# Kernel optimization log

Hardware: AMD Instinct MI355X
Metric: run time of the kernel (lower is better)

Reference implementation:

```python
import jax, jax.numpy as jnp
import numpy as np

NP_CONST = 48.0  # Np in the original code


def dft_matrices(freq=48, time=512):
    # A[t, f] = exp(-2j*pi*t*f/time)/sqrt(time), split into re/im, shape [time, freq]
    t = np.arange(time)[:, None]
    f = np.arange(freq)[None, :]
    ang = -2.0 * np.pi * t * f / time
    scale = 1.0 / np.sqrt(time)
    return (np.cos(ang) * scale).astype(np.float32), (np.sin(ang) * scale).astype(np.float32)


def _mm(xr, xi, wr, wi):
    # complex matmul: (xr + i xi) @ (wr + i wi)
    return xr @ wr - xi @ wi, xr @ wi + xi @ wr


def _act(R, sigma, theta):
    # scaled soft-threshold (standard LAMP shrinkage); returns f and df/dR
    lam = theta[0] * sigma
    mag = jnp.abs(R)
    shr = jnp.maximum(mag - lam, 0.0)
    f = theta[1] * jnp.sign(R) * shr
    df = theta[1] * (mag > lam).astype(R.dtype)
    return f, df


def setup_inputs() -> dict:
    key = jax.random.key(0)
    L, B = 8, 8192
    dre, dim = dft_matrices(48, 512)
    u = jax.random.normal(key, (B, 48, 2), dtype=jnp.float32)
    # per-layer params initialized to the DFT matrices (as in LAMP_layer.__init__)
    A_re = jnp.broadcast_to(jnp.asarray(dre), (L, 512, 48)).copy()
    A_im = jnp.broadcast_to(jnp.asarray(dim), (L, 512, 48)).copy()
    theta = jnp.broadcast_to(jnp.array([1.0, 1.0, -1.0], dtype=jnp.float32), (L, 3)).copy()
    return {"u": u, "A_re": A_re, "A_im": A_im, "theta": theta,
            "DFT_re": jnp.asarray(dre), "DFT_im": jnp.asarray(dim)}


def _lamp_forward(u, A_re, A_im, theta, DFT_re, DFT_im):
    u_re, u_im = u[:, :, 0], u[:, :, 1]          # [B, 48]
    B = u_re.shape[0]
    z_re, z_im = u_re, u_im
    H_re = jnp.zeros((B, 512), dtype=u.dtype)
    H_im = jnp.zeros((B, 512), dtype=u.dtype)

    def layer(carry, params):
        z_re, z_im, H_re, H_im = carry
        Are, Aim, th = params                      # [512,48], [512,48], [3]
        # Z = z @ A.T : [B,48] x [48,512]
        Z_re, Z_im = _mm(z_re, z_im, Are.T, Aim.T)
        R_re = H_re + Z_re
        R_im = H_im + Z_im
        sigma = jnp.sqrt(jnp.sum(z_re * z_re) + jnp.sum(z_im * z_im)) / jnp.sqrt(NP_CONST)
        Hn_re, d_re = _act(R_re, sigma, th)
        Hn_im, d_im = _act(R_im, sigma, th)
        b_re = d_re.sum() / NP_CONST
        b_im = d_im.sum() / NP_CONST
        # h_hat = H_hat @ A : [B,512] x [512,48]
        h_re, h_im = _mm(Hn_re, Hn_im, Are, Aim)
        zn_re = u_re - h_re + b_re * z_re
        zn_im = u_im - h_im + b_im * z_im
        return (zn_re, zn_im, Hn_re, Hn_im), None

    (z_re, z_im, H_re, H_im), _ = jax.lax.scan(layer, (z_re, z_im, H_re, H_im),
                                               (A_re, A_im, theta))
    h_re, h_im = _mm(H_re, H_im, DFT_re, DFT_im)   # [B, 48]
    return jnp.stack((h_re, h_im), axis=2)          # [B, 48, 2]


def reference(u, A_re, A_im, theta, DFT_re, DFT_im):
    return _lamp_forward(u, A_re, A_im, theta, DFT_re, DFT_im)
```

## Files before the change

kernel.cpp:

```cpp
#include <hip/hip_runtime.h>
#include <hip/hip_bf16.h>
#include <math.h>

#define B_   8192
#define F_   48
#define T_   512
#define L_   8
#define NBLK 256
#define THR  512
#define NW   8
#define RPB  32
#define HST  520
#define ZS   52

typedef unsigned short ushort_t;
typedef unsigned int   uint_t;
typedef __attribute__((ext_vector_type(8))) short short8;
typedef __attribute__((ext_vector_type(4))) float f32x4;

#define MFMA(a,b,c) __builtin_amdgcn_mfma_f32_16x16x32_bf16(a,b,c,0,0,0)

__device__ inline ushort_t f2bf(float x) {
    __hip_bfloat16 h = __float2bfloat16(x);
    return *reinterpret_cast<ushort_t*>(&h);
}
__device__ inline short8 negbf(short8 v) {
    short8 r;
    #pragma unroll
    for (int i = 0; i < 8; ++i) r[i] = v[i] ^ (short)0x8000;
    return r;
}
__device__ inline short8 pack8(float4 a, float4 b) {
    short8 r;
    r[0]=(short)f2bf(a.x); r[1]=(short)f2bf(a.y); r[2]=(short)f2bf(a.z); r[3]=(short)f2bf(a.w);
    r[4]=(short)f2bf(b.x); r[5]=(short)f2bf(b.y); r[6]=(short)f2bf(b.z); r[7]=(short)f2bf(b.w);
    return r;
}

__device__ inline void bar_add(uint_t* cnt) {
    __hip_atomic_fetch_add(cnt, 1u, __ATOMIC_RELEASE, __HIP_MEMORY_SCOPE_AGENT);
}
__device__ inline void bar_wait(uint_t* cnt, uint_t tgt) {
    if (threadIdx.x == 0) {
        while (__hip_atomic_load(cnt, __ATOMIC_RELAXED, __HIP_MEMORY_SCOPE_AGENT) < tgt)
            __builtin_amdgcn_s_sleep(2);
        (void)__hip_atomic_load(cnt, __ATOMIC_ACQUIRE, __HIP_MEMORY_SCOPE_AGENT);
    }
    __syncthreads();
}
__device__ inline float aload(const float* p) {
    return __hip_atomic_load(p, __ATOMIC_RELAXED, __HIP_MEMORY_SCOPE_AGENT);
}
__device__ inline void afadd(float* p, float v) {
    (void)__hip_atomic_fetch_add(p, v, __ATOMIC_RELAXED, __HIP_MEMORY_SCOPE_AGENT);
}

__global__ __launch_bounds__(256) void k_pre(
    const float* __restrict__ Ar, const float* __restrict__ Ai,
    const float* __restrict__ Dr, const float* __restrict__ Di,
    ushort_t* __restrict__ Afr, ushort_t* __restrict__ Afi,
    ushort_t* __restrict__ Atr, ushort_t* __restrict__ Ati,
    ushort_t* __restrict__ Dfr, ushort_t* __restrict__ Dfi,
    float* __restrict__ slots, uint_t* __restrict__ cnt)
{
    const int gt = blockIdx.x * 256 + threadIdx.x;
    const int gs = gridDim.x * 256;
    if (gt == 0) *cnt = 0u;
    if (gt < 32) slots[gt] = 0.f;
    for (int idx = gt; idx < L_ * 32768; idx += gs) {
        int j = idx & 7, rest = idx >> 3;
        int mm = rest & 15; rest >>= 4;
        int qq = rest & 3;  rest >>= 2;
        int k2 = rest & 1;  rest >>= 1;
        int tile = rest & 31;
        int l = rest >> 5;
        int t = tile * 16 + mm, k = k2 * 32 + qq * 8 + j;
        float vr = 0.f, vi = 0.f;
        if (k < 48) { int g = l * 24576 + t * 48 + k; vr = Ar[g]; vi = Ai[g]; }
        Afr[idx] = f2bf(vr); Afi[idx] = f2bf(vi);
    }
    for (int idx = gt; idx < L_ * 24576; idx += gs) {
        int j = idx & 7, rest = idx >> 3;
        int mm = rest & 15; rest >>= 4;
        int qq = rest & 3;  rest >>= 2;
        int ks = rest & 15; rest >>= 4;
        int ft = rest % 3;
        int l = rest / 3;
        int f = ft * 16 + mm, k = ks * 32 + qq * 8 + j;
        int g = l * 24576 + k * 48 + f;
        Atr[idx] = f2bf(Ar[g]); Ati[idx] = f2bf(Ai[g]);
    }
    for (int idx = gt; idx < 24576; idx += gs) {
        int j = idx & 7, rest = idx >> 3;
        int mm = rest & 15; rest >>= 4;
        int qq = rest & 3;  rest >>= 2;
        int ks = rest & 15;
        int ft = rest >> 4;
        int f = ft * 16 + mm, k = ks * 32 + qq * 8 + j;
        Dfr[idx] = f2bf(Dr[k * 48 + f]); Dfi[idx] = f2bf(Di[k * 48 + f]);
    }
}

__global__ __launch_bounds__(THR, 2) void k_lamp(
    const float* __restrict__ u,
    const ushort_t* __restrict__ Afr, const ushort_t* __restrict__ Afi,
    const ushort_t* __restrict__ Atr, const ushort_t* __restrict__ Ati,
    const ushort_t* __restrict__ Dfr, const ushort_t* __restrict__ Dfi,
    const float* __restrict__ th,
    float* slots, uint_t* cnt,
    float* __restrict__ out)
{
    extern __shared__ char dyn[];
    float*    pR   = (float*)dyn;
    float*    pI   = pR + 8 * 3 * 16 * 17;
    float*    zreL = pI + 8 * 3 * 16 * 17;
    float*    zimL = zreL + RPB * ZS;
    float*    red8 = zimL + RPB * ZS;
    ushort_t* HreL = (ushort_t*)(red8 + 16);
    ushort_t* HimL = HreL + RPB * HST;

    const int tid = threadIdx.x, blk = blockIdx.x;
    const int row0 = blk * RPB;
    const int wave = tid >> 6, lane = tid & 63;
    const int quad = lane >> 4, m = lane & 15;
    const int rows16 = (wave >> 2) * 16;
    const int rt = wave >> 2, kq = wave & 3;
    const float2* u2 = (const float2*)u;
    float* sigS = slots;
    float* brS  = slots + 8;
    float* biS  = slots + 16;
    uint_t tgt = 0;

    f32x4 hR[8], hI[8];
    #pragma unroll
    for (int ct = 0; ct < 8; ++ct) { hR[ct] = (f32x4){0,0,0,0}; hI[ct] = (f32x4){0,0,0,0}; }

    float acc = 0.f;
    #pragma unroll
    for (int k3 = 0; k3 < 3; ++k3) {
        int j = tid + k3 * THR;
        int r = j / 48, c = j - r * 48;
        float2 v = u2[(row0 + r) * 48 + c];
        zreL[r * ZS + c] = v.x; zimL[r * ZS + c] = v.y;
        acc += v.x * v.x + v.y * v.y;
    }
    #pragma unroll
    for (int s = 32; s > 0; s >>= 1) acc += __shfl_xor(acc, s, 64);
    __syncthreads();
    if ((tid & 63) == 0) red8[tid >> 6] = acc;
    __syncthreads();
    if (tid == 0) {
        float t = 0.f;
        #pragma unroll
        for (int w = 0; w < NW; ++w) t += red8[w];
        afadd(&sigS[0], t); bar_add(cnt);
    }
    tgt += NBLK;

    for (int l = 0; l < L_; ++l) {
        const float* zpr = zreL + (rows16 + m) * ZS;
        const float* zpi = zimL + (rows16 + m) * ZS;
        short8 zr0 = pack8(*(const float4*)(zpr + quad * 8), *(const float4*)(zpr + quad * 8 + 4));
        short8 zi0 = pack8(*(const float4*)(zpi + quad * 8), *(const float4*)(zpi + quad * 8 + 4));
        short8 zr1 = {0,0,0,0,0,0,0,0}, zi1 = {0,0,0,0,0,0,0,0};
        if (quad < 2) {
            zr1 = pack8(*(const float4*)(zpr + 32 + quad * 8), *(const float4*)(zpr + 36 + quad * 8));
            zi1 = pack8(*(const float4*)(zpi + 32 + quad * 8), *(const float4*)(zpi + 36 + quad * 8));
        }
        short8 zin0 = negbf(zi0), zin1 = negbf(zi1);

        const ushort_t* Aflr = Afr + (size_t)l * 32768;
        const ushort_t* Afli = Afi + (size_t)l * 32768;
        #pragma unroll
        for (int ct = 0; ct < 8; ++ct) {
            const int tile = (wave & 3) * 8 + ct;
            const ushort_t* rp = Aflr + (size_t)(tile * 2) * 512 + lane * 8;
            const ushort_t* ip = Afli + (size_t)(tile * 2) * 512 + lane * 8;
            short8 ar0 = *(const short8*)rp;
            short8 ar1 = *(const short8*)(rp + 512);
            short8 ai0 = *(const short8*)ip;
            short8 ai1 = *(const short8*)(ip + 512);
            hR[ct] = MFMA(zr0, ar0, hR[ct]);
            hR[ct] = MFMA(zr1, ar1, hR[ct]);
            hR[ct] = MFMA(zin0, ai0, hR[ct]);
            hR[ct] = MFMA(zin1, ai1, hR[ct]);
            hI[ct] = MFMA(zr0, ai0, hI[ct]);
            hI[ct] = MFMA(zr1, ai1, hI[ct]);
            hI[ct] = MFMA(zi0, ar0, hI[ct]);
            hI[ct] = MFMA(zi1, ar1, hI[ct]);
        }

        bar_wait(cnt, tgt);
        const float lam = th[l * 3] * sqrtf(aload(&sigS[l]) * (1.0f / 48.0f));
        const float th1 = th[l * 3 + 1];

        float cr = 0.f, ci = 0.f;
        #pragma unroll
        for (int ct = 0; ct < 8; ++ct) {
            const int t = ((wave & 3) * 8 + ct) * 16 + m;
            #pragma unroll
            for (int reg = 0; reg < 4; ++reg) {
                const int lr = rows16 + quad * 4 + reg;
                float Rr = hR[ct][reg], Ri = hI[ct][reg];
                float mr = fabsf(Rr), mi = fabsf(Ri);
                float fr = th1 * copysignf(fmaxf(mr - lam, 0.f), Rr);
                float fi = th1 * copysignf(fmaxf(mi - lam, 0.f), Ri);
                cr += (mr > lam) ? 1.f : 0.f;
                ci += (mi > lam) ? 1.f : 0.f;
                hR[ct][reg] = fr; hI[ct][reg] = fi;
                HreL[lr * HST + t] = f2bf(fr);
                HimL[lr * HST + t] = f2bf(fi);
            }
        }

        if (l == L_ - 1) { __syncthreads(); break; }

        #pragma unroll
        for (int s = 32; s > 0; s >>= 1) { cr += __shfl_xor(cr, s, 64); ci += __shfl_xor(ci, s, 64); }
        __syncthreads();
        if ((tid & 63) == 0) { red8[tid >> 6] = cr; red8[8 + (tid >> 6)] = ci; }
        __syncthreads();
        if (tid == 0) {
            float tr = 0.f, tii = 0.f;
            #pragma unroll
            for (int w = 0; w < NW; ++w) { tr += red8[w]; tii += red8[8 + w]; }
            afadd(&brS[l], tr); afadd(&biS[l], tii); bar_add(cnt);
        }
        tgt += NBLK;

        const ushort_t* Atlr = Atr + (size_t)l * 24576;
        const ushort_t* Atli = Ati + (size_t)l * 24576;
        f32x4 aR[3], aI[3];
        #pragma unroll
        for (int q = 0; q < 3; ++q) { aR[q] = (f32x4){0,0,0,0}; aI[q] = (f32x4){0,0,0,0}; }
        #pragma unroll
        for (int ks = 0; ks < 4; ++ks) {
            const int ksa = kq * 4 + ks;
            const int k0 = ksa * 32 + quad * 8;
            short8 hr = *(const short8*)&HreL[(rt * 16 + m) * HST + k0];
            short8 hi = *(const short8*)&HimL[(rt * 16 + m) * HST + k0];
            short8 hin = negbf(hi);
            #pragma unroll
            for (int ft = 0; ft < 3; ++ft) {
                short8 br = *(const short8*)(Atlr + (size_t)((ft * 16 + ksa) * 64 + lane) * 8);
                short8 bi = *(const short8*)(Atli + (size_t)((ft * 16 + ksa) * 64 + lane) * 8);
                aR[ft] = MFMA(hr, br, aR[ft]);
                aR[ft] = MFMA(hin, bi, aR[ft]);
                aI[ft] = MFMA(hr, bi, aI[ft]);
                aI[ft] = MFMA(hi, br, aI[ft]);
            }
        }
        #pragma unroll
        for (int ft = 0; ft < 3; ++ft) {
            #pragma unroll
            for (int reg = 0; reg < 4; ++reg) {
                pR[((wave * 3 + ft) * 16 + quad * 4 + reg) * 17 + m] = aR[ft][reg];
                pI[((wave * 3 + ft) * 16 + quad * 4 + reg) * 17 + m] = aI[ft][reg];
            }
        }

        bar_wait(cnt, tgt);
        const float bre = th1 * aload(&brS[l]) * (1.0f / 48.0f);
        const float bim = th1 * aload(&biS[l]) * (1.0f / 48.0f);

        float nrm = 0.f;
        #pragma unroll
        for (int k3 = 0; k3 < 3; ++k3) {
            int j = tid + k3 * THR;
            int r = j / 48, f = j - r * 48;
            int rt2 = r >> 4, lr = r & 15, ft = f >> 4, c = f & 15;
            float hRv = 0.f, hIv = 0.f;
            #pragma unroll
            for (int q = 0; q < 4; ++q) {
                hRv += pR[(((rt2 * 4 + q) * 3 + ft) * 16 + lr) * 17 + c];
                hIv += pI[(((rt2 * 4 + q) * 3 + ft) * 16 + lr) * 17 + c];
            }
            float2 uv = u2[(row0 + r) * 48 + f];
            float zr = zreL[r * ZS + f], zi = zimL[r * ZS + f];
            float znr = uv.x - hRv + bre * zr;
            float zni = uv.y - hIv + bim * zi;
            zreL[r * ZS + f] = znr; zimL[r * ZS + f] = zni;
            nrm += znr * znr + zni * zni;
        }
        #pragma unroll
        for (int s = 32; s > 0; s >>= 1) nrm += __shfl_xor(nrm, s, 64);
        __syncthreads();
        if ((tid & 63) == 0) red8[tid >> 6] = nrm;
        __syncthreads();
        if (tid == 0) {
            float t = 0.f;
            #pragma unroll
            for (int w = 0; w < NW; ++w) t += red8[w];
            afadd(&sigS[l + 1], t); bar_add(cnt);
        }
        tgt += NBLK;
    }

    f32x4 fR[3], fI[3];
    #pragma unroll
    for (int q = 0; q < 3; ++q) { fR[q] = (f32x4){0,0,0,0}; fI[q] = (f32x4){0,0,0,0}; }
    #pragma unroll
    for (int ks = 0; ks < 4; ++ks) {
        const int ksa = kq * 4 + ks;
        const int k0 = ksa * 32 + quad * 8;
        short8 hr = *(const short8*)&HreL[(rt * 16 + m) * HST + k0];
        short8 hi = *(const short8*)&HimL[(rt * 16 + m) * HST + k0];
        short8 hin = negbf(hi);
        #pragma unroll
        for (int ft = 0; ft < 3; ++ft) {
            short8 br = *(const short8*)(Dfr + (size_t)((ft * 16 + ksa) * 64 + lane) * 8);
            short8 bi = *(const short8*)(Dfi + (size_t)((ft * 16 + ksa) * 64 + lane) * 8);
            fR[ft] = MFMA(hr, br, fR[ft]);
            fR[ft] = MFMA(hin, bi, fR[ft]);
            fI[ft] = MFMA(hr, bi, fI[ft]);
            fI[ft] = MFMA(hi, br, fI[ft]);
        }
    }
    #pragma unroll
    for (int ft = 0; ft < 3; ++ft) {
        #pragma unroll
        for (int reg = 0; reg < 4; ++reg) {
            pR[((wave * 3 + ft) * 16 + quad * 4 + reg) * 17 + m] = fR[ft][reg];
            pI[((wave * 3 + ft) * 16 + quad * 4 + reg) * 17 + m] = fI[ft][reg];
        }
    }
    __syncthreads();
    float2* out2 = (float2*)out;
    #pragma unroll
    for (int k3 = 0; k3 < 3; ++k3) {
        int j = tid + k3 * THR;
        int r = j / 48, f = j - r * 48;
        int rt2 = r >> 4, lr = r & 15, ft = f >> 4, c = f & 15;
        float hRv = 0.f, hIv = 0.f;
        #pragma unroll
        for (int q = 0; q < 4; ++q) {
            hRv += pR[(((rt2 * 4 + q) * 3 + ft) * 16 + lr) * 17 + c];
            hIv += pI[(((rt2 * 4 + q) * 3 + ft) * 16 + lr) * 17 + c];
        }
        out2[(row0 + r) * 48 + f] = make_float2(hRv, hIv);
    }
}

extern "C" void kernel_launch(void* const* d_in, const int* in_sizes, int n_in,
                              void* d_out, int out_size, void* d_ws, size_t ws_size,
                              hipStream_t stream) {
    (void)in_sizes; (void)n_in; (void)out_size; (void)ws_size;
    const float* u  = (const float*)d_in[0];
    const float* Ar = (const float*)d_in[1];
    const float* Ai = (const float*)d_in[2];
    const float* th = (const float*)d_in[3];
    const float* Dr = (const float*)d_in[4];
    const float* Di = (const float*)d_in[5];
    float* out = (float*)d_out;

    char* p = (char*)d_ws;
    auto alloc = [&](size_t bytes) -> char* {
        char* r = p;
        p += (bytes + 255) & ~(size_t)255;
        return r;
    };
    float*    slots = (float*)alloc(32 * 4);
    uint_t*   cnt   = (uint_t*)alloc(64);
    ushort_t* Afr = (ushort_t*)alloc((size_t)L_ * 32768 * 2);
    ushort_t* Afi = (ushort_t*)alloc((size_t)L_ * 32768 * 2);
    ushort_t* Atr = (ushort_t*)alloc((size_t)L_ * 24576 * 2);
    ushort_t* Ati = (ushort_t*)alloc((size_t)L_ * 24576 * 2);
    ushort_t* Dfr = (ushort_t*)alloc((size_t)24576 * 2);
    ushort_t* Dfi = (ushort_t*)alloc((size_t)24576 * 2);

    k_pre<<<1024, 256, 0, stream>>>(Ar, Ai, Dr, Di, Afr, Afi, Atr, Ati, Dfr, Dfi, slots, cnt);

    const uint_t lds_bytes = 132160;
    hipFuncSetAttribute((const void*)k_lamp,
                        hipFuncAttributeMaxDynamicSharedMemorySize, (int)lds_bytes);
    void* args[] = { (void*)&u, (void*)&Afr, (void*)&Afi, (void*)&Atr, (void*)&Ati,
                     (void*)&Dfr, (void*)&Dfi, (void*)&th,
                     (void*)&slots, (void*)&cnt, (void*)&out };
    hipLaunchCooperativeKernel((void*)k_lamp, dim3(NBLK), dim3(THR), args,
                               lds_bytes, stream);
}
```

Before: 261.8 us.

## Replace single-counter grid barrier with striped counters and leader broadcast

```diff
diff --git a/kernel.cpp b/kernel.cpp
--- a/kernel.cpp
+++ b/kernel.cpp
@@ -12,6 +12,7 @@
 #define RPB  32
 #define HST  520
 #define ZS   52
+#define LINE 32
 
 typedef unsigned short ushort_t;
 typedef unsigned int   uint_t;
@@ -37,23 +38,64 @@
     return r;
 }
 
-__device__ inline void bar_add(uint_t* cnt) {
-    __hip_atomic_fetch_add(cnt, 1u, __ATOMIC_RELEASE, __HIP_MEMORY_SCOPE_AGENT);
-}
-__device__ inline void bar_wait(uint_t* cnt, uint_t tgt) {
-    if (threadIdx.x == 0) {
-        while (__hip_atomic_load(cnt, __ATOMIC_RELAXED, __HIP_MEMORY_SCOPE_AGENT) < tgt)
-            __builtin_amdgcn_s_sleep(2);
-        (void)__hip_atomic_load(cnt, __ATOMIC_ACQUIRE, __HIP_MEMORY_SCOPE_AGENT);
-    }
-    __syncthreads();
-}
 __device__ inline float aload(const float* p) {
     return __hip_atomic_load(p, __ATOMIC_RELAXED, __HIP_MEMORY_SCOPE_AGENT);
 }
+__device__ inline void astore(float* p, float v) {
+    __hip_atomic_store(p, v, __ATOMIC_RELAXED, __HIP_MEMORY_SCOPE_AGENT);
+}
 __device__ inline void afadd(float* p, float v) {
     (void)__hip_atomic_fetch_add(p, v, __ATOMIC_RELAXED, __HIP_MEMORY_SCOPE_AGENT);
 }
+
+__device__ inline void arrive(float* vbase, uint_t* cnt8, int blk,
+                              float v0, float v1, int nv) {
+    afadd(vbase + (blk & 7) * LINE, v0);
+    if (nv > 1) afadd(vbase + (8 + (blk & 7)) * LINE, v1);
+    (void)__hip_atomic_fetch_add(&cnt8[(blk & 7) * LINE], 1u,
+                                 __ATOMIC_RELEASE, __HIP_MEMORY_SCOPE_AGENT);
+}
+
+__device__ inline float2 collect(uint_t* cnt8, float* vbase, float* bcbase,
+                                 uint_t target, int nv) {
+    for (;;) {
+        uint_t s = 0;
+        #pragma unroll
+        for (int i = 0; i < 8; ++i)
+            s += __hip_atomic_load(&cnt8[i * LINE], __ATOMIC_RELAXED, __HIP_MEMORY_SCOPE_AGENT);
+        if (s >= target) break;
+        __builtin_amdgcn_s_sleep(1);
+    }
+    (void)__hip_atomic_load(&cnt8[0], __ATOMIC_ACQUIRE, __HIP_MEMORY_SCOPE_AGENT);
+    float v0 = 0.f, v1 = 0.f;
+    #pragma unroll
+    for (int i = 0; i < 8; ++i) v0 += aload(vbase + i * LINE);
+    if (nv > 1) {
+        #pragma unroll
+        for (int i = 0; i < 8; ++i) v1 += aload(vbase + (8 + i) * LINE);
+    }
+    #pragma unroll
+    for (int j = 0; j < 8; ++j) {
+        astore(bcbase + j * LINE + 1, v0);
+        astore(bcbase + j * LINE + 2, v1);
+    }
+    #pragma unroll
+    for (int j = 0; j < 8; ++j)
+        __hip_atomic_store((uint_t*)(bcbase + j * LINE), 1u,
+                           __ATOMIC_RELEASE, __HIP_MEMORY_SCOPE_AGENT);
+    return make_float2(v0, v1);
+}
+
+__device__ inline float2 waitbc(const float* bcline) {
+    while (__hip_atomic_load((const uint_t*)bcline, __ATOMIC_RELAXED,
+                             __HIP_MEMORY_SCOPE_AGENT) == 0u)
+        __builtin_amdgcn_s_sleep(2);
+    (void)__hip_atomic_load((const uint_t*)bcline, __ATOMIC_ACQUIRE,
+                            __HIP_MEMORY_SCOPE_AGENT);
+    return make_float2(aload(bcline + 1), aload(bcline + 2));
+}
+
+#define SYNC_DW ((8 + 16 * 8 + 16 * 16) * LINE)
 
 __global__ __launch_bounds__(256) void k_pre(
     const float* __restrict__ Ar, const float* __restrict__ Ai,
@@ -61,12 +103,11 @@
     ushort_t* __restrict__ Afr, ushort_t* __restrict__ Afi,
     ushort_t* __restrict__ Atr, ushort_t* __restrict__ Ati,
     ushort_t* __restrict__ Dfr, ushort_t* __restrict__ Dfi,
-    float* __restrict__ slots, uint_t* __restrict__ cnt)
+    uint_t* __restrict__ syncbuf)
 {
     const int gt = blockIdx.x * 256 + threadIdx.x;
     const int gs = gridDim.x * 256;
-    if (gt == 0) *cnt = 0u;
-    if (gt < 32) slots[gt] = 0.f;
+    for (int idx = gt; idx < SYNC_DW; idx += gs) syncbuf[idx] = 0u;
     for (int idx = gt; idx < L_ * 32768; idx += gs) {
         int j = idx & 7, rest = idx >> 3;
         int mm = rest & 15; rest >>= 4;
@@ -107,7 +148,7 @@
     const ushort_t* __restrict__ Atr, const ushort_t* __restrict__ Ati,
     const ushort_t* __restrict__ Dfr, const ushort_t* __restrict__ Dfi,
     const float* __restrict__ th,
-    float* slots, uint_t* cnt,
+    uint_t* syncbuf,
     float* __restrict__ out)
 {
     extern __shared__ char dyn[];
@@ -115,9 +156,13 @@
     float*    pI   = pR + 8 * 3 * 16 * 17;
     float*    zreL = pI + 8 * 3 * 16 * 17;
     float*    zimL = zreL + RPB * ZS;
-    float*    red8 = zimL + RPB * ZS;
-    ushort_t* HreL = (ushort_t*)(red8 + 16);
+    float*    red  = zimL + RPB * ZS;
+    ushort_t* HreL = (ushort_t*)(red + 32);
     ushort_t* HimL = HreL + RPB * HST;
+
+    uint_t* cnt8 = syncbuf;
+    float*  bcF  = (float*)(syncbuf + 8 * LINE);
+    float*  vals = bcF + 16 * 8 * LINE;
 
     const int tid = threadIdx.x, blk = blockIdx.x;
     const int row0 = blk * RPB;
@@ -126,10 +171,18 @@
     const int rows16 = (wave >> 2) * 16;
     const int rt = wave >> 2, kq = wave & 3;
     const float2* u2 = (const float2*)u;
-    float* sigS = slots;
-    float* brS  = slots + 8;
-    float* biS  = slots + 16;
-    uint_t tgt = 0;
+
+    auto gsync = [&](int s, int nv) {
+        if (tid == 0) {
+            float2 v = (blk == 0)
+                ? collect(cnt8, vals + s * 16 * LINE, bcF + s * 8 * LINE,
+                          (uint_t)NBLK * (uint_t)(s + 1), nv)
+                : waitbc(bcF + s * 8 * LINE + (blk & 7) * LINE);
+            red[0] = v.x; red[1] = v.y;
+        }
+        __syncthreads();
+        return make_float2(red[0], red[1]);
+    };
 
     f32x4 hR[8], hI[8];
     #pragma unroll
@@ -147,15 +200,14 @@
     #pragma unroll
     for (int s = 32; s > 0; s >>= 1) acc += __shfl_xor(acc, s, 64);
     __syncthreads();
-    if ((tid & 63) == 0) red8[tid >> 6] = acc;
+    if (lane == 0) red[8 + wave] = acc;
     __syncthreads();
     if (tid == 0) {
         float t = 0.f;
         #pragma unroll
-        for (int w = 0; w < NW; ++w) t += red8[w];
-        afadd(&sigS[0], t); bar_add(cnt);
-    }
-    tgt += NBLK;
+        for (int w = 0; w < NW; ++w) t += red[8 + w];
+        arrive(vals + 0, cnt8, blk, t, 0.f, 1);
+    }
 
     for (int l = 0; l < L_; ++l) {
         const float* zpr = zreL + (rows16 + m) * ZS;
@@ -190,8 +242,8 @@
             hI[ct] = MFMA(zi1, ar1, hI[ct]);
         }
 
-        bar_wait(cnt, tgt);
-        const float lam = th[l * 3] * sqrtf(aload(&sigS[l]) * (1.0f / 48.0f));
+        float2 sv = gsync(2 * l, 1);
+        const float lam = th[l * 3] * sqrtf(sv.x * (1.0f / 48.0f));
         const float th1 = th[l * 3 + 1];
 
         float cr = 0.f, ci = 0.f;
@@ -218,15 +270,14 @@
         #pragma unroll
         for (int s = 32; s > 0; s >>= 1) { cr += __shfl_xor(cr, s, 64); ci += __shfl_xor(ci, s, 64); }
         __syncthreads();
-        if ((tid & 63) == 0) { red8[tid >> 6] = cr; red8[8 + (tid >> 6)] = ci; }
+        if (lane == 0) { red[8 + wave] = cr; red[16 + wave] = ci; }
         __syncthreads();
         if (tid == 0) {
             float tr = 0.f, tii = 0.f;
             #pragma unroll
-            for (int w = 0; w < NW; ++w) { tr += red8[w]; tii += red8[8 + w]; }
-            afadd(&brS[l], tr); afadd(&biS[l], tii); bar_add(cnt);
-        }
-        tgt += NBLK;
+            for (int w = 0; w < NW; ++w) { tr += red[8 + w]; tii += red[16 + w]; }
+            arrive(vals + (2 * l + 1) * 16 * LINE, cnt8, blk, tr, tii, 2);
+        }
 
         const ushort_t* Atlr = Atr + (size_t)l * 24576;
         const ushort_t* Atli = Ati + (size_t)l * 24576;
@@ -259,9 +310,9 @@
             }
         }
 
-        bar_wait(cnt, tgt);
-        const float bre = th1 * aload(&brS[l]) * (1.0f / 48.0f);
-        const float bim = th1 * aload(&biS[l]) * (1.0f / 48.0f);
+        float2 bv = gsync(2 * l + 1, 2);
+        const float bre = th1 * bv.x * (1.0f / 48.0f);
+        const float bim = th1 * bv.y * (1.0f / 48.0f);
 
         float nrm = 0.f;
         #pragma unroll
@@ -285,15 +336,14 @@
         #pragma unroll
         for (int s = 32; s > 0; s >>= 1) nrm += __shfl_xor(nrm, s, 64);
         __syncthreads();
-        if ((tid & 63) == 0) red8[tid >> 6] = nrm;
+        if (lane == 0) red[8 + wave] = nrm;
         __syncthreads();
         if (tid == 0) {
             float t = 0.f;
             #pragma unroll
-            for (int w = 0; w < NW; ++w) t += red8[w];
-            afadd(&sigS[l + 1], t); bar_add(cnt);
-        }
-        tgt += NBLK;
+            for (int w = 0; w < NW; ++w) t += red[8 + w];
+            arrive(vals + (2 * l + 2) * 16 * LINE, cnt8, blk, t, 0.f, 1);
+        }
     }
 
     f32x4 fR[3], fI[3];
@@ -359,8 +409,7 @@
         p += (bytes + 255) & ~(size_t)255;
         return r;
     };
-    float*    slots = (float*)alloc(32 * 4);
-    uint_t*   cnt   = (uint_t*)alloc(64);
+    uint_t*   syncbuf = (uint_t*)alloc(SYNC_DW * 4);
     ushort_t* Afr = (ushort_t*)alloc((size_t)L_ * 32768 * 2);
     ushort_t* Afi = (ushort_t*)alloc((size_t)L_ * 32768 * 2);
     ushort_t* Atr = (ushort_t*)alloc((size_t)L_ * 24576 * 2);
@@ -368,14 +417,14 @@
     ushort_t* Dfr = (ushort_t*)alloc((size_t)24576 * 2);
     ushort_t* Dfi = (ushort_t*)alloc((size_t)24576 * 2);
 
-    k_pre<<<1024, 256, 0, stream>>>(Ar, Ai, Dr, Di, Afr, Afi, Atr, Ati, Dfr, Dfi, slots, cnt);
-
-    const uint_t lds_bytes = 132160;
+    k_pre<<<1024, 256, 0, stream>>>(Ar, Ai, Dr, Di, Afr, Afi, Atr, Ati, Dfr, Dfi, syncbuf);
+
+    const uint_t lds_bytes = 132224;
     hipFuncSetAttribute((const void*)k_lamp,
                         hipFuncAttributeMaxDynamicSharedMemorySize, (int)lds_bytes);
     void* args[] = { (void*)&u, (void*)&Afr, (void*)&Afi, (void*)&Atr, (void*)&Ati,
                      (void*)&Dfr, (void*)&Dfi, (void*)&th,
-                     (void*)&slots, (void*)&cnt, (void*)&out };
+                     (void*)&syncbuf, (void*)&out };
     hipLaunchCooperativeKernel((void*)k_lamp, dim3(NBLK), dim3(THR), args,
                                lds_bytes, stream);
 }
```

New measurement: 290.2 us. 1.11x slower.
